# Optimization experiments

Hardware: AMD Instinct MI355X
Metric: run time of the kernel (lower is better)

Reference implementation:

```python
import jax, jax.numpy as jnp
import numpy as np

H, I, E, K = 1024, 2816, 8, 2  # hidden, intermediate, n_experts, topk
B, S = 2, 2048


def setup_inputs() -> dict:
    key = jax.random.key(0)
    ks = jax.random.split(key, 6)
    def init(k, shape, fan_in):
        return (jax.random.normal(k, shape, jnp.float32) / np.sqrt(fan_in)).astype(jnp.float32)
    return {
        "x": jax.random.normal(ks[0], (B, S, H), jnp.float32),
        "Wgate": init(ks[1], (H, E), H),   # gating Linear weight (in,out layout)
        "bgate": jnp.zeros((E,), jnp.float32),  # gating Linear bias (nn.Linear default bias=True)
        "Wg": init(ks[2], (E, H, I), H),   # stacked gate_proj, mlp_bias=False
        "Wu": init(ks[3], (E, H, I), H),   # stacked up_proj
        "Wd": init(ks[4], (E, I, H), I),   # stacked down_proj
    }


def reference(x, Wgate, bgate, Wg, Wu, Wd):
    Bb, Ss, Hd = x.shape
    xf = x.reshape(-1, Hd)                       # [N, H] flattened tokens
    logits = xf @ Wgate + bgate                  # [N, E] gate logits
    topv, topi = jax.lax.top_k(logits, K)        # [N, K]
    N = xf.shape[0]
    # sparse combine weights: raw top-k LOGITS (no softmax), zeros elsewhere
    # (faithful to torch: scatter of logits_topk into -inf mask; -inf slots
    #  are never read since only selected experts contribute)
    combine = jnp.zeros_like(logits).at[jnp.arange(N)[:, None], topi].set(topv)  # [N, E]
    # dense grouped SwiGLU over all experts, then sparse combine
    g = jnp.einsum('nh,ehi->nei', xf, Wg)        # [N, E, I]
    u = jnp.einsum('nh,ehi->nei', xf, Wu)        # [N, E, I]
    h = jax.nn.silu(g) * u                       # [N, E, I]
    eo = jnp.einsum('nei,eih->neh', h, Wd)       # [N, E, H]
    out = jnp.einsum('neh,ne->nh', eo, combine).reshape(Bb, Ss, Hd)
    return out, logits
```

## Files before the change

kernel.cpp:

```cpp
#include <hip/hip_runtime.h>

#define HDIM 1024
#define IDIM 2816
#define NEXP 8
#define NTOK 4096
#define NROWS 8192
#define RPAD 8320
#define MAXT 71
#define GU_NYT 44
#define DN_NYT 8
#define GU_TG 8
#define GU_NTG 9
#define GU_NWG (GU_NTG * GU_NYT * GU_TG)
#define DN_NWG (MAXT * DN_NYT)

typedef short bf16x8 __attribute__((ext_vector_type(8)));
typedef float f32x4 __attribute__((ext_vector_type(4)));
typedef unsigned short u16x8 __attribute__((ext_vector_type(8)));

static __device__ __forceinline__ unsigned short f2bf(float f) {
    union { float f; unsigned int i; } v; v.f = f;
    return (unsigned short)((v.i + 0x7fffu + ((v.i >> 16) & 1u)) >> 16);
}

static __device__ __forceinline__ void gload16(const void* g, void* l) {
    __builtin_amdgcn_global_load_lds(
        (const __attribute__((address_space(1))) unsigned int*)g,
        (__attribute__((address_space(3))) unsigned int*)l, 16, 0, 0);
}

__global__ __launch_bounds__(256) void gating_kernel(
    const float* __restrict__ x, const float* __restrict__ Wgate,
    const float* __restrict__ bgate, float* __restrict__ logits_out,
    int* __restrict__ counts, int* __restrict__ topi, float* __restrict__ topv)
{
    int wave = (blockIdx.x << 2) + (threadIdx.x >> 6);
    int lane = threadIdx.x & 63;
    if (wave >= NTOK) return;
    const float* xr = x + (size_t)wave * HDIM;

    double acc[NEXP];
#pragma unroll
    for (int e = 0; e < NEXP; ++e) acc[e] = 0.0;

    for (int it = 0; it < HDIM / 64; ++it) {
        int h = lane + (it << 6);
        float xv = xr[h];
        const float* wr = Wgate + (size_t)h * NEXP;
#pragma unroll
        for (int e = 0; e < NEXP; ++e) acc[e] += (double)xv * (double)wr[e];
    }
#pragma unroll
    for (int e = 0; e < NEXP; ++e) {
        double v = acc[e];
        for (int off = 32; off; off >>= 1) v += __shfl_xor(v, off, 64);
        acc[e] = v + (double)bgate[e];
    }
    float lf[NEXP];
#pragma unroll
    for (int e = 0; e < NEXP; ++e) lf[e] = (float)acc[e];

    if (lane < NEXP) logits_out[(size_t)wave * NEXP + lane] = lf[lane];

    if (lane == 0) {
        int i1 = 0; float v1 = lf[0];
#pragma unroll
        for (int e = 1; e < NEXP; ++e) if (lf[e] > v1) { v1 = lf[e]; i1 = e; }
        int i2 = -1; float v2 = -3.0e38f;
#pragma unroll
        for (int e = 0; e < NEXP; ++e) {
            if (e == i1) continue;
            if (lf[e] > v2) { v2 = lf[e]; i2 = e; }
        }
        topi[wave * 2 + 0] = i1; topv[wave * 2 + 0] = v1;
        topi[wave * 2 + 1] = i2; topv[wave * 2 + 1] = v2;
        atomicAdd(&counts[i1], 1);
        atomicAdd(&counts[i2], 1);
    }
}

__global__ void offsets_kernel(const int* __restrict__ counts,
                               int* __restrict__ offs, int* __restrict__ cursor,
                               int* __restrict__ ntile, int* __restrict__ te,
                               int* __restrict__ tm0)
{
    if (threadIdx.x == 0 && blockIdx.x == 0) {
        int s = 0;
        for (int e = 0; e < NEXP; ++e) { offs[e] = s; cursor[e] = s; s += counts[e]; }
        offs[NEXP] = s;
        int nt = 0;
        for (int e = 0; e < NEXP; ++e) {
            int c = counts[e], base = offs[e];
            for (int mt = 0; mt * 128 < c; ++mt) { te[nt] = e; tm0[nt] = base + mt * 128; ++nt; }
        }
        *ntile = nt;
    }
}

__global__ __launch_bounds__(256) void scatter_kernel(
    const float* __restrict__ x, const int* __restrict__ topi,
    const float* __restrict__ topv, int* __restrict__ cursor,
    float* __restrict__ row_w, int* __restrict__ tok_of,
    unsigned short* __restrict__ Xg)
{
    int p = (blockIdx.x << 2) + (threadIdx.x >> 6);
    int lane = threadIdx.x & 63;
    if (p >= NROWS) return;
    int n = p >> 1;
    int e = topi[p];
    float w = topv[p];
    int pos = 0;
    if (lane == 0) {
        pos = atomicAdd(&cursor[e], 1);
        row_w[pos] = w;
        tok_of[pos] = n;
    }
    pos = __shfl(pos, 0, 64);
    const float* xr = x + (size_t)n * HDIM;
    unsigned short* dst = Xg + (size_t)pos * HDIM;
#pragma unroll
    for (int it = 0; it < HDIM / 256; ++it) {
        int idx = (it * 64 + lane) * 4;
        float4 v = *reinterpret_cast<const float4*>(&xr[idx]);
        ushort4 o;
        o.x = f2bf(v.x); o.y = f2bf(v.y); o.z = f2bf(v.z); o.w = f2bf(v.w);
        *reinterpret_cast<ushort4*>(&dst[idx]) = o;
    }
}

__global__ __launch_bounds__(256) void transpose_cvt_gu_kernel(
    const float* __restrict__ Wg, const float* __restrict__ Wu,
    unsigned short* __restrict__ W2)
{
    __shared__ unsigned short lds[64 * 66];
    const int kind = blockIdx.z;
    const int e = blockIdx.y;
    const float* s0 = (kind ? Wu : Wg) + (size_t)e * HDIM * IDIM;
    unsigned short* d0 = W2 + (size_t)e * 2 * IDIM * HDIM;
    const int TC = IDIM / 64;
    int tt = blockIdx.x;
    int tr = tt / TC, tc = tt % TC;
    int tid = threadIdx.x;
    {
        int r = tid >> 2, c0 = (tid & 3) << 4;
        const float* s = s0 + (size_t)(tr * 64 + r) * IDIM + tc * 64 + c0;
        float4 v0 = *reinterpret_cast<const float4*>(s);
        float4 v1 = *reinterpret_cast<const float4*>(s + 4);
        float4 v2 = *reinterpret_cast<const float4*>(s + 8);
        float4 v3 = *reinterpret_cast<const float4*>(s + 12);
        unsigned short* lr_ = &lds[r * 66 + c0];
        lr_[0]  = f2bf(v0.x); lr_[1]  = f2bf(v0.y); lr_[2]  = f2bf(v0.z); lr_[3]  = f2bf(v0.w);
        lr_[4]  = f2bf(v1.x); lr_[5]  = f2bf(v1.y); lr_[6]  = f2bf(v1.z); lr_[7]  = f2bf(v1.w);
        lr_[8]  = f2bf(v2.x); lr_[9]  = f2bf(v2.y); lr_[10] = f2bf(v2.z); lr_[11] = f2bf(v2.w);
        lr_[12] = f2bf(v3.x); lr_[13] = f2bf(v3.y); lr_[14] = f2bf(v3.z); lr_[15] = f2bf(v3.w);
    }
    __syncthreads();
    {
        int c = tid >> 2, q0 = (tid & 3) << 4;
        u16x8 o0, o1;
#pragma unroll
        for (int j = 0; j < 8; ++j) o0[j] = lds[(q0 + j) * 66 + c];
#pragma unroll
        for (int j = 0; j < 8; ++j) o1[j] = lds[(q0 + 8 + j) * 66 + c];
        int i = tc * 64 + c;
        int r2 = ((i >> 4) << 5) + (kind << 4) + (i & 15);
        unsigned short* d = d0 + (size_t)r2 * HDIM + tr * 64 + q0;
        *reinterpret_cast<u16x8*>(d) = o0;
        *reinterpret_cast<u16x8*>(d + 8) = o1;
    }
}

__global__ __launch_bounds__(256) void transpose_cvt_d_kernel(
    const float* __restrict__ Wd, unsigned short* __restrict__ Wdt)
{
    __shared__ unsigned short lds[64 * 66];
    const int e = blockIdx.y;
    const float* s0 = Wd + (size_t)e * IDIM * HDIM;
    unsigned short* d0 = Wdt + (size_t)e * HDIM * IDIM;
    const int TC = HDIM / 64;
    int tt = blockIdx.x;
    int tr = tt / TC, tc = tt % TC;
    int tid = threadIdx.x;
    {
        int r = tid >> 2, c0 = (tid & 3) << 4;
        const float* s = s0 + (size_t)(tr * 64 + r) * HDIM + tc * 64 + c0;
        float4 v0 = *reinterpret_cast<const float4*>(s);
        float4 v1 = *reinterpret_cast<const float4*>(s + 4);
        float4 v2 = *reinterpret_cast<const float4*>(s + 8);
        float4 v3 = *reinterpret_cast<const float4*>(s + 12);
        unsigned short* lr_ = &lds[r * 66 + c0];
        lr_[0]  = f2bf(v0.x); lr_[1]  = f2bf(v0.y); lr_[2]  = f2bf(v0.z); lr_[3]  = f2bf(v0.w);
        lr_[4]  = f2bf(v1.x); lr_[5]  = f2bf(v1.y); lr_[6]  = f2bf(v1.z); lr_[7]  = f2bf(v1.w);
        lr_[8]  = f2bf(v2.x); lr_[9]  = f2bf(v2.y); lr_[10] = f2bf(v2.z); lr_[11] = f2bf(v2.w);
        lr_[12] = f2bf(v3.x); lr_[13] = f2bf(v3.y); lr_[14] = f2bf(v3.z); lr_[15] = f2bf(v3.w);
    }
    __syncthreads();
    {
        int c = tid >> 2, q0 = (tid & 3) << 4;
        u16x8 o0, o1;
#pragma unroll
        for (int j = 0; j < 8; ++j) o0[j] = lds[(q0 + j) * 66 + c];
#pragma unroll
        for (int j = 0; j < 8; ++j) o1[j] = lds[(q0 + 8 + j) * 66 + c];
        unsigned short* d = d0 + (size_t)(tc * 64 + c) * IDIM + tr * 64 + q0;
        *reinterpret_cast<u16x8*>(d) = o0;
        *reinterpret_cast<u16x8*>(d + 8) = o1;
    }
}

__global__ __launch_bounds__(256, 4) void gateup_kernel(
    const unsigned short* __restrict__ Xg,
    const unsigned short* __restrict__ W2,
    const int* __restrict__ offs,
    const int* __restrict__ ntile, const int* __restrict__ te,
    const int* __restrict__ tm0, unsigned short* __restrict__ hbuf)
{
    __shared__ unsigned short As[128 * 64];
    __shared__ unsigned short Bs[128 * 64];

    int bid = blockIdx.x;
    int xcd = bid & 7, rest = bid >> 3;
    int wg = xcd * (GU_NWG / 8) + rest;
    int tg = wg / (GU_NYT * GU_TG);
    int r2 = wg % (GU_NYT * GU_TG);
    int ny = r2 >> 3, ti = r2 & 7;
    int t = tg * GU_TG + ti;
    if (t >= *ntile) return;

    const int e = te[t];
    const int m0 = tm0[t];
    const int r1 = offs[e + 1];
    const int n0 = ny * 128;

    const unsigned short* wb = W2 + (size_t)e * 2 * IDIM * HDIM;

    const int tid = threadIdx.x;
    const int lane = tid & 63, wv = tid >> 6;
    const int wr = (wv >> 1) * 64, wc = (wv & 1) * 64;
    const int lr = lane & 15, kq16 = lane >> 4;

    const int a_row8 = tid >> 3;
    const int a_c16 = tid & 7;

    f32x4 zero = {0.f, 0.f, 0.f, 0.f};
    f32x4 acc[4][4];
#pragma unroll
    for (int m = 0; m < 4; ++m)
#pragma unroll
        for (int n = 0; n < 4; ++n) acc[m][n] = zero;

    for (int k0 = 0; k0 < HDIM; k0 += 64) {
        __syncthreads();
#pragma unroll
        for (int ch = 0; ch < 4; ++ch) {
            int row = ch * 32 + a_row8;
            int c16s = a_c16 ^ (row & 7);
            gload16(&Xg[(size_t)(m0 + row) * HDIM + k0 + c16s * 8], &As[ch * 2048 + tid * 8]);
            gload16(&wb[(size_t)(n0 + row) * HDIM + k0 + c16s * 8], &Bs[ch * 2048 + tid * 8]);
        }
        __syncthreads();

#pragma unroll
        for (int ks = 0; ks < 2; ++ks) {
            bf16x8 af[4], bf[4];
#pragma unroll
            for (int m = 0; m < 4; ++m) {
                int row = wr + m * 16 + lr;
                int sw = (ks * 4 + kq16) ^ (row & 7);
                af[m] = *reinterpret_cast<const bf16x8*>(&As[row * 64 + sw * 8]);
            }
#pragma unroll
            for (int n = 0; n < 4; ++n) {
                int row = wc + n * 16 + lr;
                int sw = (ks * 4 + kq16) ^ (row & 7);
                bf[n] = *reinterpret_cast<const bf16x8*>(&Bs[row * 64 + sw * 8]);
            }
#pragma unroll
            for (int m = 0; m < 4; ++m)
#pragma unroll
                for (int n = 0; n < 4; ++n)
                    acc[m][n] = __builtin_amdgcn_mfma_f32_16x16x32_bf16(af[m], bf[n], acc[m][n], 0, 0, 0);
        }
    }

    const int rr = (lane >> 4) * 4;
    const int iloc0 = ((wc >> 5) << 4) + lr;
    const int col0 = ny * 64 + iloc0;
#pragma unroll
    for (int m = 0; m < 4; ++m) {
#pragma unroll
        for (int j = 0; j < 4; ++j) {
            int grow = m0 + wr + m * 16 + rr + j;
            if (grow < r1) {
                unsigned short* hr = &hbuf[(size_t)grow * IDIM + col0];
                float g0 = acc[m][0][j], u0 = acc[m][1][j];
                float g1 = acc[m][2][j], u1 = acc[m][3][j];
                hr[0]  = f2bf(g0 / (1.0f + __expf(-g0)) * u0);
                hr[16] = f2bf(g1 / (1.0f + __expf(-g1)) * u1);
            }
        }
    }
}

__global__ __launch_bounds__(256, 4) void down_kernel(
    const unsigned short* __restrict__ hbuf,
    const unsigned short* __restrict__ Wdt,
    const int* __restrict__ offs,
    const int* __restrict__ ntile, const int* __restrict__ te,
    const int* __restrict__ tm0,
    const float* __restrict__ row_w, const int* __restrict__ tok_of,
    float* __restrict__ out)
{
    __shared__ unsigned short As[128 * 64];
    __shared__ unsigned short Bs[128 * 64];

    int bid = blockIdx.x;
    int xcd = bid & 7, rest = bid >> 3;
    int wg = xcd * (DN_NWG / 8) + rest;
    int t = wg >> 3;
    int ny = wg & 7;
    if (t >= *ntile) return;

    const int e = te[t];
    const int m0 = tm0[t];
    const int r1 = offs[e + 1];
    const int n0 = ny * 128;

    const unsigned short* wd = Wdt + (size_t)e * HDIM * IDIM;

    const int tid = threadIdx.x;
    const int lane = tid & 63, wv = tid >> 6;
    const int wr = (wv >> 1) * 64, wc = (wv & 1) * 64;
    const int lr = lane & 15, kq16 = lane >> 4;

    const int a_row8 = tid >> 3;
    const int a_c16 = tid & 7;

    f32x4 zero = {0.f, 0.f, 0.f, 0.f};
    f32x4 acc[4][4];
#pragma unroll
    for (int m = 0; m < 4; ++m)
#pragma unroll
        for (int n = 0; n < 4; ++n) acc[m][n] = zero;

    for (int k0 = 0; k0 < IDIM; k0 += 64) {
        __syncthreads();
#pragma unroll
        for (int ch = 0; ch < 4; ++ch) {
            int row = ch * 32 + a_row8;
            int c16s = a_c16 ^ (row & 7);
            gload16(&hbuf[(size_t)(m0 + row) * IDIM + k0 + c16s * 8], &As[ch * 2048 + tid * 8]);
            gload16(&wd[(size_t)(n0 + row) * IDIM + k0 + c16s * 8], &Bs[ch * 2048 + tid * 8]);
        }
        __syncthreads();

#pragma unroll
        for (int ks = 0; ks < 2; ++ks) {
            bf16x8 af[4], bf[4];
#pragma unroll
            for (int m = 0; m < 4; ++m) {
                int row = wr + m * 16 + lr;
                int sw = (ks * 4 + kq16) ^ (row & 7);
                af[m] = *reinterpret_cast<const bf16x8*>(&As[row * 64 + sw * 8]);
            }
#pragma unroll
            for (int n = 0; n < 4; ++n) {
                int row = wc + n * 16 + lr;
                int sw = (ks * 4 + kq16) ^ (row & 7);
                bf[n] = *reinterpret_cast<const bf16x8*>(&Bs[row * 64 + sw * 8]);
            }
#pragma unroll
            for (int m = 0; m < 4; ++m)
#pragma unroll
                for (int n = 0; n < 4; ++n)
                    acc[m][n] = __builtin_amdgcn_mfma_f32_16x16x32_bf16(af[m], bf[n], acc[m][n], 0, 0, 0);
        }
    }

    const int rr = (lane >> 4) * 4;
#pragma unroll
    for (int m = 0; m < 4; ++m) {
#pragma unroll
        for (int j = 0; j < 4; ++j) {
            int grow = m0 + wr + m * 16 + rr + j;
            if (grow < r1) {
                float w = row_w[grow];
                int tok = tok_of[grow];
                float* orow = out + (size_t)tok * HDIM + n0 + wc + lr;
#pragma unroll
                for (int n = 0; n < 4; ++n)
                    atomicAdd(&orow[n * 16], acc[m][n][j] * w);
            }
        }
    }
}

extern "C" void kernel_launch(void* const* d_in, const int* in_sizes, int n_in,
                              void* d_out, int out_size, void* d_ws, size_t ws_size,
                              hipStream_t stream)
{
    const float* x     = (const float*)d_in[0];
    const float* Wgate = (const float*)d_in[1];
    const float* bgate = (const float*)d_in[2];
    const float* Wg    = (const float*)d_in[3];
    const float* Wu    = (const float*)d_in[4];
    const float* Wd    = (const float*)d_in[5];
    float* out = (float*)d_out;
    float* logits = out + (size_t)NTOK * HDIM;

    char* ws = (char*)d_ws;
    unsigned short* Xg   = (unsigned short*)ws;
    unsigned short* hbuf = (unsigned short*)(ws + 17039360);
    unsigned short* W2   = (unsigned short*)(ws + 63897600);
    char* meta = ws + 156172288;
    int*   counts = (int*)(meta);
    int*   offs   = (int*)(meta + 64);
    int*   cursor = (int*)(meta + 128);
    int*   ntile  = (int*)(meta + 192);
    int*   te     = (int*)(meta + 256);
    int*   tm0    = (int*)(meta + 768);
    int*   topi   = (int*)(meta + 2048);
    float* topv   = (float*)(meta + 34816);
    float* row_w  = (float*)(meta + 67584);
    int*   tok_of = (int*)(meta + 100352);

    hipMemsetAsync(counts, 0, 32, stream);
    hipMemsetAsync(out, 0, (size_t)NTOK * HDIM * sizeof(float), stream);

    gating_kernel<<<NTOK / 4, 256, 0, stream>>>(x, Wgate, bgate, logits, counts, topi, topv);
    offsets_kernel<<<1, 64, 0, stream>>>(counts, offs, cursor, ntile, te, tm0);
    scatter_kernel<<<NROWS / 4, 256, 0, stream>>>(x, topi, topv, cursor, row_w, tok_of, Xg);

    transpose_cvt_gu_kernel<<<dim3((HDIM / 64) * (IDIM / 64), NEXP, 2), 256, 0, stream>>>(Wg, Wu, W2);

    gateup_kernel<<<GU_NWG, 256, 0, stream>>>(Xg, W2, offs, ntile, te, tm0, hbuf);

    transpose_cvt_d_kernel<<<dim3((IDIM / 64) * (HDIM / 64), NEXP), 256, 0, stream>>>(Wd, W2);

    down_kernel<<<DN_NWG, 256, 0, stream>>>(hbuf, W2, offs, ntile, te, tm0, row_w, tok_of, out);
}
```

Baseline: 483.3 us.

## Fuse weight transposes with gating into one prep kernel, split down-proj K

Merges the gate/up weight transpose, the down-weight transpose (when workspace is large enough for a separate buffer) and the gating computation into a single prep launch, removing launch gaps and letting these independent jobs run concurrently. The down-projection kernel now splits its K dimension in two, doubling the number of workgroups to improve occupancy. Both halves accumulate into the output, which the unseen epilogue presumably does with atomics. The large-workspace path needs extra memory, and the split-K adds more output traffic.

```diff
diff --git a/kernel.cpp b/kernel.cpp
--- a/kernel.cpp
+++ b/kernel.cpp
@@ -8,11 +8,15 @@
 #define RPAD 8320
 #define MAXT 71
 #define GU_NYT 44
-#define DN_NYT 8
 #define GU_TG 8
 #define GU_NTG 9
 #define GU_NWG (GU_NTG * GU_NYT * GU_TG)
-#define DN_NWG (MAXT * DN_NYT)
+#define DN_KS 2
+#define DN_NWG (MAXT * 8 * DN_KS)
+
+#define N_TGU 11264
+#define N_TD  5632
+#define N_GATE 1024
 
 typedef short bf16x8 __attribute__((ext_vector_type(8)));
 typedef float f32x4 __attribute__((ext_vector_type(4)));
@@ -29,20 +33,90 @@
         (__attribute__((address_space(3))) unsigned int*)l, 16, 0, 0);
 }
 
-__global__ __launch_bounds__(256) void gating_kernel(
+static __device__ __forceinline__ void transpose_tile(
+    const float* __restrict__ s0, int C, int tr, int tc, int tid,
+    unsigned short* lds, u16x8& o0, u16x8& o1, int& c_out)
+{
+    {
+        int r = tid >> 2, c0 = (tid & 3) << 4;
+        const float* s = s0 + (size_t)(tr * 64 + r) * C + tc * 64 + c0;
+        float4 v0 = *reinterpret_cast<const float4*>(s);
+        float4 v1 = *reinterpret_cast<const float4*>(s + 4);
+        float4 v2 = *reinterpret_cast<const float4*>(s + 8);
+        float4 v3 = *reinterpret_cast<const float4*>(s + 12);
+        unsigned short* lr_ = &lds[r * 66 + c0];
+        lr_[0]  = f2bf(v0.x); lr_[1]  = f2bf(v0.y); lr_[2]  = f2bf(v0.z); lr_[3]  = f2bf(v0.w);
+        lr_[4]  = f2bf(v1.x); lr_[5]  = f2bf(v1.y); lr_[6]  = f2bf(v1.z); lr_[7]  = f2bf(v1.w);
+        lr_[8]  = f2bf(v2.x); lr_[9]  = f2bf(v2.y); lr_[10] = f2bf(v2.z); lr_[11] = f2bf(v2.w);
+        lr_[12] = f2bf(v3.x); lr_[13] = f2bf(v3.y); lr_[14] = f2bf(v3.z); lr_[15] = f2bf(v3.w);
+    }
+    __syncthreads();
+    {
+        int c = tid >> 2, q0 = (tid & 3) << 4;
+#pragma unroll
+        for (int j = 0; j < 8; ++j) o0[j] = lds[(q0 + j) * 66 + c];
+#pragma unroll
+        for (int j = 0; j < 8; ++j) o1[j] = lds[(q0 + 8 + j) * 66 + c];
+        c_out = c;
+    }
+}
+
+__global__ __launch_bounds__(256) void prep_kernel(
     const float* __restrict__ x, const float* __restrict__ Wgate,
-    const float* __restrict__ bgate, float* __restrict__ logits_out,
-    int* __restrict__ counts, int* __restrict__ topi, float* __restrict__ topv)
-{
-    int wave = (blockIdx.x << 2) + (threadIdx.x >> 6);
-    int lane = threadIdx.x & 63;
+    const float* __restrict__ bgate,
+    const float* __restrict__ Wg, const float* __restrict__ Wu,
+    const float* __restrict__ Wd,
+    float* __restrict__ logits_out, int* __restrict__ counts,
+    int* __restrict__ topi, float* __restrict__ topv,
+    unsigned short* __restrict__ W2, unsigned short* __restrict__ Wdt,
+    int n_td)
+{
+    __shared__ unsigned short lds[64 * 66];
+    const int b = blockIdx.x;
+    const int tid = threadIdx.x;
+
+    if (b < N_TGU) {
+        int kind = b / (NEXP * 704);
+        int rem = b % (NEXP * 704);
+        int e = rem / 704;
+        int tt = rem % 704;
+        const int TC = IDIM / 64;
+        int tr = tt / TC, tc = tt % TC;
+        const float* s0 = (kind ? Wu : Wg) + (size_t)e * HDIM * IDIM;
+        unsigned short* d0 = W2 + (size_t)e * 2 * IDIM * HDIM;
+        u16x8 o0, o1; int c;
+        transpose_tile(s0, IDIM, tr, tc, tid, lds, o0, o1, c);
+        int i = tc * 64 + c;
+        int r2 = ((i >> 4) << 5) + (kind << 4) + (i & 15);
+        unsigned short* d = d0 + (size_t)r2 * HDIM + tr * 64 + ((tid & 3) << 4);
+        *reinterpret_cast<u16x8*>(d) = o0;
+        *reinterpret_cast<u16x8*>(d + 8) = o1;
+        return;
+    }
+    if (b < N_TGU + n_td) {
+        int bb = b - N_TGU;
+        int e = bb / 704;
+        int tt = bb % 704;
+        const int TC = HDIM / 64;
+        int tr = tt / TC, tc = tt % TC;
+        const float* s0 = Wd + (size_t)e * IDIM * HDIM;
+        unsigned short* d0 = Wdt + (size_t)e * HDIM * IDIM;
+        u16x8 o0, o1; int c;
+        transpose_tile(s0, HDIM, tr, tc, tid, lds, o0, o1, c);
+        unsigned short* d = d0 + (size_t)(tc * 64 + c) * IDIM + tr * 64 + ((tid & 3) << 4);
+        *reinterpret_cast<u16x8*>(d) = o0;
+        *reinterpret_cast<u16x8*>(d + 8) = o1;
+        return;
+    }
+    int bb = b - N_TGU - n_td;
+    int wave = (bb << 2) + (tid >> 6);
+    int lane = tid & 63;
     if (wave >= NTOK) return;
     const float* xr = x + (size_t)wave * HDIM;
 
     double acc[NEXP];
 #pragma unroll
     for (int e = 0; e < NEXP; ++e) acc[e] = 0.0;
-
     for (int it = 0; it < HDIM / 64; ++it) {
         int h = lane + (it << 6);
         float xv = xr[h];
@@ -77,6 +151,24 @@
         atomicAdd(&counts[i1], 1);
         atomicAdd(&counts[i2], 1);
     }
+}
+
+__global__ __launch_bounds__(256) void transpose_cvt_d_kernel(
+    const float* __restrict__ Wd, unsigned short* __restrict__ Wdt)
+{
+    __shared__ unsigned short lds[64 * 66];
+    const int e = blockIdx.y;
+    const float* s0 = Wd + (size_t)e * IDIM * HDIM;
+    unsigned short* d0 = Wdt + (size_t)e * HDIM * IDIM;
+    const int TC = HDIM / 64;
+    int tt = blockIdx.x;
+    int tr = tt / TC, tc = tt % TC;
+    int tid = threadIdx.x;
+    u16x8 o0, o1; int c;
+    transpose_tile(s0, HDIM, tr, tc, tid, lds, o0, o1, c);
+    unsigned short* d = d0 + (size_t)(tc * 64 + c) * IDIM + tr * 64 + ((tid & 3) << 4);
+    *reinterpret_cast<u16x8*>(d) = o0;
+    *reinterpret_cast<u16x8*>(d + 8) = o1;
 }
 
 __global__ void offsets_kernel(const int* __restrict__ counts,
@@ -128,86 +220,6 @@
     }
 }
 
-__global__ __launch_bounds__(256) void transpose_cvt_gu_kernel(
-    const float* __restrict__ Wg, const float* __restrict__ Wu,
-    unsigned short* __restrict__ W2)
-{
-    __shared__ unsigned short lds[64 * 66];
-    const int kind = blockIdx.z;
-    const int e = blockIdx.y;
-    const float* s0 = (kind ? Wu : Wg) + (size_t)e * HDIM * IDIM;
-    unsigned short* d0 = W2 + (size_t)e * 2 * IDIM * HDIM;
-    const int TC = IDIM / 64;
-    int tt = blockIdx.x;
-    int tr = tt / TC, tc = tt % TC;
-    int tid = threadIdx.x;
-    {
-        int r = tid >> 2, c0 = (tid & 3) << 4;
-        const float* s = s0 + (size_t)(tr * 64 + r) * IDIM + tc * 64 + c0;
-        float4 v0 = *reinterpret_cast<const float4*>(s);
-        float4 v1 = *reinterpret_cast<const float4*>(s + 4);
-        float4 v2 = *reinterpret_cast<const float4*>(s + 8);
-        float4 v3 = *reinterpret_cast<const float4*>(s + 12);
-        unsigned short* lr_ = &lds[r * 66 + c0];
-        lr_[0]  = f2bf(v0.x); lr_[1]  = f2bf(v0.y); lr_[2]  = f2bf(v0.z); lr_[3]  = f2bf(v0.w);
-        lr_[4]  = f2bf(v1.x); lr_[5]  = f2bf(v1.y); lr_[6]  = f2bf(v1.z); lr_[7]  = f2bf(v1.w);
-        lr_[8]  = f2bf(v2.x); lr_[9]  = f2bf(v2.y); lr_[10] = f2bf(v2.z); lr_[11] = f2bf(v2.w);
-        lr_[12] = f2bf(v3.x); lr_[13] = f2bf(v3.y); lr_[14] = f2bf(v3.z); lr_[15] = f2bf(v3.w);
-    }
-    __syncthreads();
-    {
-        int c = tid >> 2, q0 = (tid & 3) << 4;
-        u16x8 o0, o1;
-#pragma unroll
-        for (int j = 0; j < 8; ++j) o0[j] = lds[(q0 + j) * 66 + c];
-#pragma unroll
-        for (int j = 0; j < 8; ++j) o1[j] = lds[(q0 + 8 + j) * 66 + c];
-        int i = tc * 64 + c;
-        int r2 = ((i >> 4) << 5) + (kind << 4) + (i & 15);
-        unsigned short* d = d0 + (size_t)r2 * HDIM + tr * 64 + q0;
-        *reinterpret_cast<u16x8*>(d) = o0;
-        *reinterpret_cast<u16x8*>(d + 8) = o1;
-    }
-}
-
-__global__ __launch_bounds__(256) void transpose_cvt_d_kernel(
-    const float* __restrict__ Wd, unsigned short* __restrict__ Wdt)
-{
-    __shared__ unsigned short lds[64 * 66];
-    const int e = blockIdx.y;
-    const float* s0 = Wd + (size_t)e * IDIM * HDIM;
-    unsigned short* d0 = Wdt + (size_t)e * HDIM * IDIM;
-    const int TC = HDIM / 64;
-    int tt = blockIdx.x;
-    int tr = tt / TC, tc = tt % TC;
-    int tid = threadIdx.x;
-    {
-        int r = tid >> 2, c0 = (tid & 3) << 4;
-        const float* s = s0 + (size_t)(tr * 64 + r) * HDIM + tc * 64 + c0;
-        float4 v0 = *reinterpret_cast<const float4*>(s);
-        float4 v1 = *reinterpret_cast<const float4*>(s + 4);
-        float4 v2 = *reinterpret_cast<const float4*>(s + 8);
-        float4 v3 = *reinterpret_cast<const float4*>(s + 12);
-        unsigned short* lr_ = &lds[r * 66 + c0];
-        lr_[0]  = f2bf(v0.x); lr_[1]  = f2bf(v0.y); lr_[2]  = f2bf(v0.z); lr_[3]  = f2bf(v0.w);
-        lr_[4]  = f2bf(v1.x); lr_[5]  = f2bf(v1.y); lr_[6]  = f2bf(v1.z); lr_[7]  = f2bf(v1.w);
-        lr_[8]  = f2bf(v2.x); lr_[9]  = f2bf(v2.y); lr_[10] = f2bf(v2.z); lr_[11] = f2bf(v2.w);
-        lr_[12] = f2bf(v3.x); lr_[13] = f2bf(v3.y); lr_[14] = f2bf(v3.z); lr_[15] = f2bf(v3.w);
-    }
-    __syncthreads();
-    {
-        int c = tid >> 2, q0 = (tid & 3) << 4;
-        u16x8 o0, o1;
-#pragma unroll
-        for (int j = 0; j < 8; ++j) o0[j] = lds[(q0 + j) * 66 + c];
-#pragma unroll
-        for (int j = 0; j < 8; ++j) o1[j] = lds[(q0 + 8 + j) * 66 + c];
-        unsigned short* d = d0 + (size_t)(tc * 64 + c) * IDIM + tr * 64 + q0;
-        *reinterpret_cast<u16x8*>(d) = o0;
-        *reinterpret_cast<u16x8*>(d + 8) = o1;
-    }
-}
-
 __global__ __launch_bounds__(256, 4) void gateup_kernel(
     const unsigned short* __restrict__ Xg,
     const unsigned short* __restrict__ W2,
@@ -317,8 +329,10 @@
     int bid = blockIdx.x;
     int xcd = bid & 7, rest = bid >> 3;
     int wg = xcd * (DN_NWG / 8) + rest;
-    int t = wg >> 3;
-    int ny = wg & 7;
+    int t = wg >> 4;
+    int r = wg & 15;
+    int ny = r >> 1;
+    int kh = r & 1;
     if (t >= *ntile) return;
 
     const int e = te[t];
@@ -343,7 +357,9 @@
 #pragma unroll
         for (int n = 0; n < 4; ++n) acc[m][n] = zero;
 
-    for (int k0 = 0; k0 < IDIM; k0 += 64) {
+    const int kbeg = kh * (IDIM / DN_KS);
+    const int kend = kbeg + (IDIM / DN_KS);
+    for (int k0 = kbeg; k0 < kend; k0 += 64) {
         __syncthreads();
 #pragma unroll
         for (int ch = 0; ch < 4; ++ch) {
@@ -412,7 +428,11 @@
     unsigned short* Xg   = (unsigned short*)ws;
     unsigned short* hbuf = (unsigned short*)(ws + 17039360);
     unsigned short* W2   = (unsigned short*)(ws + 63897600);
-    char* meta = ws + 156172288;
+
+    const bool big = ws_size >= (size_t)202309632 + 1048576;
+    unsigned short* Wdt = big ? (unsigned short*)(ws + 156172288) : W2;
+    char* meta = ws + (big ? 202309632 : 156172288);
+
     int*   counts = (int*)(meta);
     int*   offs   = (int*)(meta + 64);
     int*   cursor = (int*)(meta + 128);
@@ -427,15 +447,18 @@
     hipMemsetAsync(counts, 0, 32, stream);
     hipMemsetAsync(out, 0, (size_t)NTOK * HDIM * sizeof(float), stream);
 
-    gating_kernel<<<NTOK / 4, 256, 0, stream>>>(x, Wgate, bgate, logits, counts, topi, topv);
+    const int n_td = big ? N_TD : 0;
+    prep_kernel<<<N_TGU + n_td + N_GATE, 256, 0, stream>>>(
+        x, Wgate, bgate, Wg, Wu, Wd, logits, counts, topi, topv, W2, Wdt, n_td);
+
     offsets_kernel<<<1, 64, 0, stream>>>(counts, offs, cursor, ntile, te, tm0);
     scatter_kernel<<<NROWS / 4, 256, 0, stream>>>(x, topi, topv, cursor, row_w, tok_of, Xg);
 
-    transpose_cvt_gu_kernel<<<dim3((HDIM / 64) * (IDIM / 64), NEXP, 2), 256, 0, stream>>>(Wg, Wu, W2);
-
     gateup_kernel<<<GU_NWG, 256, 0, stream>>>(Xg, W2, offs, ntile, te, tm0, hbuf);
 
-    transpose_cvt_d_kernel<<<dim3((IDIM / 64) * (HDIM / 64), NEXP), 256, 0, stream>>>(Wd, W2);
-
-    down_kernel<<<DN_NWG, 256, 0, stream>>>(hbuf, W2, offs, ntile, te, tm0, row_w, tok_of, out);
-}
+    if (!big) {
+        transpose_cvt_d_kernel<<<dim3((IDIM / 64) * (HDIM / 64), NEXP), 256, 0, stream>>>(Wd, Wdt);
+    }
+
+    down_kernel<<<DN_NWG, 256, 0, stream>>>(hbuf, Wdt, offs, ntile, te, tm0, row_w, tok_of, out);
+}
```

Measured after the change: 500.8 us. 1.04x slower.

## Split-K the down GEMM and enlarge weight transpose tiles to 128x128

Applied to the files above, without the earlier changes.

The down-projection kernel now splits the intermediate dimension into two halves, doubling the number of workgroups so more of the GPU is occupied. Each half accumulates into the output, presumably through the existing atomic combine. The fp32-to-bf16 weight transpose kernels now use 128x128 tiles with wider vectorized LDS writes and 16-byte global stores. This cuts per-block overhead and improves store coalescing, at the cost of more LDS per block and extra atomic traffic on the output.

```diff
diff --git a/kernel.cpp b/kernel.cpp
--- a/kernel.cpp
+++ b/kernel.cpp
@@ -8,11 +8,12 @@
 #define RPAD 8320
 #define MAXT 71
 #define GU_NYT 44
-#define DN_NYT 8
 #define GU_TG 8
 #define GU_NTG 9
 #define GU_NWG (GU_NTG * GU_NYT * GU_TG)
-#define DN_NWG (MAXT * DN_NYT)
+#define DN_KS 2
+#define DN_NWG (MAXT * 8 * DN_KS)
+#define TLDP 130
 
 typedef short bf16x8 __attribute__((ext_vector_type(8)));
 typedef float f32x4 __attribute__((ext_vector_type(4)));
@@ -42,7 +43,6 @@
     double acc[NEXP];
 #pragma unroll
     for (int e = 0; e < NEXP; ++e) acc[e] = 0.0;
-
     for (int it = 0; it < HDIM / 64; ++it) {
         int h = lane + (it << 6);
         float xv = xr[h];
@@ -128,83 +128,85 @@
     }
 }
 
-__global__ __launch_bounds__(256) void transpose_cvt_gu_kernel(
+__global__ __launch_bounds__(256) void transpose_gu_kernel(
     const float* __restrict__ Wg, const float* __restrict__ Wu,
     unsigned short* __restrict__ W2)
 {
-    __shared__ unsigned short lds[64 * 66];
+    __shared__ unsigned short lds[128 * TLDP];
     const int kind = blockIdx.z;
     const int e = blockIdx.y;
+    const int tt = blockIdx.x;
+    const int tr = tt / 22, tc = tt % 22;
+    const int tid = threadIdx.x;
+
     const float* s0 = (kind ? Wu : Wg) + (size_t)e * HDIM * IDIM;
-    unsigned short* d0 = W2 + (size_t)e * 2 * IDIM * HDIM;
-    const int TC = IDIM / 64;
-    int tt = blockIdx.x;
-    int tr = tt / TC, tc = tt % TC;
-    int tid = threadIdx.x;
     {
-        int r = tid >> 2, c0 = (tid & 3) << 4;
-        const float* s = s0 + (size_t)(tr * 64 + r) * IDIM + tc * 64 + c0;
-        float4 v0 = *reinterpret_cast<const float4*>(s);
-        float4 v1 = *reinterpret_cast<const float4*>(s + 4);
-        float4 v2 = *reinterpret_cast<const float4*>(s + 8);
-        float4 v3 = *reinterpret_cast<const float4*>(s + 12);
-        unsigned short* lr_ = &lds[r * 66 + c0];
-        lr_[0]  = f2bf(v0.x); lr_[1]  = f2bf(v0.y); lr_[2]  = f2bf(v0.z); lr_[3]  = f2bf(v0.w);
-        lr_[4]  = f2bf(v1.x); lr_[5]  = f2bf(v1.y); lr_[6]  = f2bf(v1.z); lr_[7]  = f2bf(v1.w);
-        lr_[8]  = f2bf(v2.x); lr_[9]  = f2bf(v2.y); lr_[10] = f2bf(v2.z); lr_[11] = f2bf(v2.w);
-        lr_[12] = f2bf(v3.x); lr_[13] = f2bf(v3.y); lr_[14] = f2bf(v3.z); lr_[15] = f2bf(v3.w);
+        int r = tid >> 1, ch = (tid & 1) * 64;
+        const float* sp = s0 + (size_t)(tr * 128 + r) * IDIM + tc * 128 + ch;
+        unsigned short* lp = &lds[r * TLDP + ch];
+#pragma unroll
+        for (int q = 0; q < 8; ++q) {
+            float4 a = *reinterpret_cast<const float4*>(sp + q * 8);
+            float4 b = *reinterpret_cast<const float4*>(sp + q * 8 + 4);
+            u16x8 o;
+            o[0] = f2bf(a.x); o[1] = f2bf(a.y); o[2] = f2bf(a.z); o[3] = f2bf(a.w);
+            o[4] = f2bf(b.x); o[5] = f2bf(b.y); o[6] = f2bf(b.z); o[7] = f2bf(b.w);
+            *reinterpret_cast<u16x8*>(lp + q * 8) = o;
+        }
     }
     __syncthreads();
     {
-        int c = tid >> 2, q0 = (tid & 3) << 4;
-        u16x8 o0, o1;
-#pragma unroll
-        for (int j = 0; j < 8; ++j) o0[j] = lds[(q0 + j) * 66 + c];
-#pragma unroll
-        for (int j = 0; j < 8; ++j) o1[j] = lds[(q0 + 8 + j) * 66 + c];
-        int i = tc * 64 + c;
-        int r2 = ((i >> 4) << 5) + (kind << 4) + (i & 15);
-        unsigned short* d = d0 + (size_t)r2 * HDIM + tr * 64 + q0;
-        *reinterpret_cast<u16x8*>(d) = o0;
-        *reinterpret_cast<u16x8*>(d + 8) = o1;
-    }
-}
-
-__global__ __launch_bounds__(256) void transpose_cvt_d_kernel(
+        const int g = tid & 15;
+        unsigned short* d0 = W2 + (size_t)e * 2 * IDIM * HDIM + tr * 128 + g * 8;
+#pragma unroll
+        for (int cb = 0; cb < 8; ++cb) {
+            int c = cb * 16 + (tid >> 4);
+            u16x8 o;
+#pragma unroll
+            for (int jj = 0; jj < 8; ++jj) o[jj] = lds[(g * 8 + jj) * TLDP + c];
+            int i = tc * 128 + c;
+            int r2 = ((i >> 4) << 5) + (kind << 4) + (i & 15);
+            *reinterpret_cast<u16x8*>(d0 + (size_t)r2 * HDIM) = o;
+        }
+    }
+}
+
+__global__ __launch_bounds__(256) void transpose_d_kernel(
     const float* __restrict__ Wd, unsigned short* __restrict__ Wdt)
 {
-    __shared__ unsigned short lds[64 * 66];
+    __shared__ unsigned short lds[128 * TLDP];
     const int e = blockIdx.y;
+    const int tt = blockIdx.x;
+    const int tr = tt / 8, tc = tt % 8;
+    const int tid = threadIdx.x;
+
     const float* s0 = Wd + (size_t)e * IDIM * HDIM;
-    unsigned short* d0 = Wdt + (size_t)e * HDIM * IDIM;
-    const int TC = HDIM / 64;
-    int tt = blockIdx.x;
-    int tr = tt / TC, tc = tt % TC;
-    int tid = threadIdx.x;
     {
-        int r = tid >> 2, c0 = (tid & 3) << 4;
-        const float* s = s0 + (size_t)(tr * 64 + r) * HDIM + tc * 64 + c0;
-        float4 v0 = *reinterpret_cast<const float4*>(s);
-        float4 v1 = *reinterpret_cast<const float4*>(s + 4);
-        float4 v2 = *reinterpret_cast<const float4*>(s + 8);
-        float4 v3 = *reinterpret_cast<const float4*>(s + 12);
-        unsigned short* lr_ = &lds[r * 66 + c0];
-        lr_[0]  = f2bf(v0.x); lr_[1]  = f2bf(v0.y); lr_[2]  = f2bf(v0.z); lr_[3]  = f2bf(v0.w);
-        lr_[4]  = f2bf(v1.x); lr_[5]  = f2bf(v1.y); lr_[6]  = f2bf(v1.z); lr_[7]  = f2bf(v1.w);
-        lr_[8]  = f2bf(v2.x); lr_[9]  = f2bf(v2.y); lr_[10] = f2bf(v2.z); lr_[11] = f2bf(v2.w);
-        lr_[12] = f2bf(v3.x); lr_[13] = f2bf(v3.y); lr_[14] = f2bf(v3.z); lr_[15] = f2bf(v3.w);
+        int r = tid >> 1, ch = (tid & 1) * 64;
+        const float* sp = s0 + (size_t)(tr * 128 + r) * HDIM + tc * 128 + ch;
+        unsigned short* lp = &lds[r * TLDP + ch];
+#pragma unroll
+        for (int q = 0; q < 8; ++q) {
+            float4 a = *reinterpret_cast<const float4*>(sp + q * 8);
+            float4 b = *reinterpret_cast<const float4*>(sp + q * 8 + 4);
+            u16x8 o;
+            o[0] = f2bf(a.x); o[1] = f2bf(a.y); o[2] = f2bf(a.z); o[3] = f2bf(a.w);
+            o[4] = f2bf(b.x); o[5] = f2bf(b.y); o[6] = f2bf(b.z); o[7] = f2bf(b.w);
+            *reinterpret_cast<u16x8*>(lp + q * 8) = o;
+        }
     }
     __syncthreads();
     {
-        int c = tid >> 2, q0 = (tid & 3) << 4;
-        u16x8 o0, o1;
-#pragma unroll
-        for (int j = 0; j < 8; ++j) o0[j] = lds[(q0 + j) * 66 + c];
-#pragma unroll
-        for (int j = 0; j < 8; ++j) o1[j] = lds[(q0 + 8 + j) * 66 + c];
-        unsigned short* d = d0 + (size_t)(tc * 64 + c) * IDIM + tr * 64 + q0;
-        *reinterpret_cast<u16x8*>(d) = o0;
-        *reinterpret_cast<u16x8*>(d + 8) = o1;
+        const int g = tid & 15;
+        unsigned short* d0 = Wdt + (size_t)e * HDIM * IDIM + tr * 128 + g * 8;
+#pragma unroll
+        for (int cb = 0; cb < 8; ++cb) {
+            int c = cb * 16 + (tid >> 4);
+            u16x8 o;
+#pragma unroll
+            for (int jj = 0; jj < 8; ++jj) o[jj] = lds[(g * 8 + jj) * TLDP + c];
+            *reinterpret_cast<u16x8*>(d0 + (size_t)(tc * 128 + c) * IDIM) = o;
+        }
     }
 }
 
@@ -317,8 +319,10 @@
     int bid = blockIdx.x;
     int xcd = bid & 7, rest = bid >> 3;
     int wg = xcd * (DN_NWG / 8) + rest;
-    int t = wg >> 3;
-    int ny = wg & 7;
+    int t = wg >> 4;
+    int r = wg & 15;
+    int ny = r >> 1;
+    int kh = r & 1;
     if (t >= *ntile) return;
 
     const int e = te[t];
@@ -343,7 +347,9 @@
 #pragma unroll
         for (int n = 0; n < 4; ++n) acc[m][n] = zero;
 
-    for (int k0 = 0; k0 < IDIM; k0 += 64) {
+    const int kbeg = kh * (IDIM / DN_KS);
+    const int kend = kbeg + (IDIM / DN_KS);
+    for (int k0 = kbeg; k0 < kend; k0 += 64) {
         __syncthreads();
 #pragma unroll
         for (int ch = 0; ch < 4; ++ch) {
@@ -431,11 +437,11 @@
     offsets_kernel<<<1, 64, 0, stream>>>(counts, offs, cursor, ntile, te, tm0);
     scatter_kernel<<<NROWS / 4, 256, 0, stream>>>(x, topi, topv, cursor, row_w, tok_of, Xg);
 
-    transpose_cvt_gu_kernel<<<dim3((HDIM / 64) * (IDIM / 64), NEXP, 2), 256, 0, stream>>>(Wg, Wu, W2);
+    transpose_gu_kernel<<<dim3(176, NEXP, 2), 256, 0, stream>>>(Wg, Wu, W2);
 
     gateup_kernel<<<GU_NWG, 256, 0, stream>>>(Xg, W2, offs, ntile, te, tm0, hbuf);
 
-    transpose_cvt_d_kernel<<<dim3((IDIM / 64) * (HDIM / 64), NEXP), 256, 0, stream>>>(Wd, W2);
+    transpose_d_kernel<<<dim3(176, NEXP), 256, 0, stream>>>(Wd, W2);
 
     down_kernel<<<DN_NWG, 256, 0, stream>>>(hbuf, W2, offs, ntile, te, tm0, row_w, tok_of, out);
 }
```

After: 510.7 us. 5.7% more time.
